# Kernel optimization log

Measured on AMD Instinct MI355X. Metric: run time of the kernel, lower is better.

## Reference

```python
import jax, jax.numpy as jnp
import numpy as np
from jax import lax

DN = ('NCHW', 'OIHW', 'NCHW')

def conv3x3(x, w, b):
    y = lax.conv_general_dilated(x, w, (1, 1), 'SAME', dimension_numbers=DN)
    return y + b[None, :, None, None]

def box_filter(x, ws):
    # depthwise WxW averaging conv, VALID after reflect pad
    C = x.shape[1]
    k = jnp.ones((C, 1, ws, ws), x.dtype) / (ws * ws)
    return lax.conv_general_dilated(x, k, (1, 1), 'VALID', feature_group_count=C,
                                    dimension_numbers=DN)

def compute_std_map(features, ws):
    N, C, H, W = features.shape
    pad = ws // 2
    fp = jnp.pad(features, ((0, 0), (0, 0), (pad, pad), (pad, pad)), mode='reflect')
    local_mean = box_filter(fp, ws)            # [N,C,H,W]
    local_mean_sq = box_filter(fp * fp, ws)
    local_var = jnp.clip(local_mean_sq - local_mean ** 2, 1e-6, None)
    if C == 4:
        cw = jax.nn.softmax(jnp.array([1.0, 1.5, 1.0, 1.5], features.dtype))
    else:
        cw = jax.nn.softmax(jnp.ones((C,), features.dtype))
    result = jnp.sum(jnp.sqrt(local_var) * cw[None, :, None, None], axis=1, keepdims=True)
    return result ** 0.8                        # [N,1,H,W]

def setup_inputs() -> dict:
    key = jax.random.key(0)
    ks = jax.random.split(key, 10)
    inp = {}
    inp['x'] = jax.random.normal(ks[0], (1, 4, 1024, 1024), jnp.float32)
    inp['w1'] = jax.random.normal(ks[1], (32, 4, 3, 3), jnp.float32) * (1.0 / np.sqrt(4 * 9))
    inp['b1'] = jax.random.normal(ks[2], (32,), jnp.float32) * 0.01
    inp['w2'] = jax.random.normal(ks[3], (16, 32, 3, 3), jnp.float32) * (1.0 / np.sqrt(32 * 9))
    inp['b2'] = jax.random.normal(ks[4], (16,), jnp.float32) * 0.01
    inp['w3'] = jax.random.normal(ks[5], (8, 16, 3, 3), jnp.float32) * (1.0 / np.sqrt(16 * 9))
    inp['b3'] = jax.random.normal(ks[6], (8,), jnp.float32) * 0.01
    inp['channel_weights'] = jnp.ones((4,), jnp.float32) / 4.0
    inp['fusion_w'] = jnp.full((1, 3, 1, 1), 1.0 / 3.0, jnp.float32) + \
        jax.random.normal(ks[7], (1, 3, 1, 1), jnp.float32) * 0.02
    inp['fusion_b'] = jnp.zeros((1,), jnp.float32)
    return inp

def reference(x, w1, b1, w2, b2, w3, b3, channel_weights, fusion_w, fusion_b):
    window_sizes = [11, 25, 49]
    # feature extractor
    f = jax.nn.leaky_relu(conv3x3(x, w1, b1), 0.2)
    f = jax.nn.leaky_relu(conv3x3(f, w2, b2), 0.2)
    f = conv3x3(f, w3, b3)                      # [B,8,H,W]
    # multi-scale std maps
    maps = jnp.concatenate([compute_std_map(f, ws) for ws in window_sizes], axis=1)  # [B,3,H,W]
    fused = jax.nn.relu(
        lax.conv_general_dilated(maps, fusion_w, (1, 1), 'VALID', dimension_numbers=DN)
        + fusion_b[None, :, None, None])        # [B,1,H,W]
    # adaptive thresholds
    std_flat = fused.reshape(-1)
    q25 = jnp.quantile(std_flat, 0.25)
    q75 = jnp.quantile(std_flat, 0.75)
    iqr75 = q75 - q25
    global_std = jnp.std(x, axis=(2, 3), keepdims=True, ddof=1)   # [B,4,1,1]
    lower = (q25 - 0.5 * iqr75) * jnp.ones_like(global_std)
    upper = (q75 + 0.5 * iqr75) * jnp.ones_like(global_std)
    gf = jnp.clip(global_std * 5.0, 0.5, 2.0)
    lower = lower * gf
    upper = upper * gf
    cwn = jax.nn.softmax(channel_weights).reshape(1, 4, 1, 1)
    channel_std = jnp.std(x * cwn, axis=(2, 3), keepdims=True, ddof=1)
    cf = jnp.clip(channel_std * 2.0, 0.8, 1.2)
    lower = lower * cf
    upper = upper * cf
    # texture mask
    q30 = jnp.quantile(std_flat, 0.3)
    q70 = jnp.quantile(std_flat, 0.7)
    lower_mean = jnp.mean(lower, axis=1, keepdims=True)           # [B,1,1,1]
    upper_mean = jnp.mean(upper, axis=1, keepdims=True)
    l_t = 0.5 * lower_mean + 0.5 * q30
    u_t = 0.5 * upper_mean + 0.5 * q70
    iqr = q70 - q30
    widen = iqr < 0.01
    l_t = jnp.where(widen, l_t - iqr, l_t)
    u_t = jnp.where(widen, u_t + iqr, u_t)
    diff = u_t - l_t
    mid0 = (l_t + u_t) / 2
    narrow = diff < 0.02
    l_t = jnp.where(narrow, mid0 - 0.01, l_t)
    u_t = jnp.where(narrow, mid0 + 0.01, u_t)
    midpoint = (l_t + u_t) / 2
    scale = u_t - l_t
    normalized = jax.nn.sigmoid(4.0 * (fused - midpoint) / scale)
    nm = jnp.mean(normalized)
    mask = jnp.where(nm > 0.65, 0.1 + 0.5 * normalized,
                     jnp.where(nm < 0.35, 0.2 + 0.5 * normalized,
                               0.15 + 0.55 * normalized))
    return mask
```

## Files before the change

kernel.cpp:

```cpp
#include <hip/hip_runtime.h>
#include <stdint.h>

constexpr int H = 1024, W = 1024;
constexpr int NPIX = H * W;
constexpr int PADM = 24;
constexpr int PROW = W + 2 * PADM;

constexpr size_t OFF_F1P   = 0;
constexpr size_t OFF_F2P   = 134217728;
constexpr size_t OFF_F3    = 0;
constexpr size_t OFF_HF    = 33554432;
constexpr size_t OFF_HF2   = 67108864;
constexpr size_t OFF_FUSED = 100663296;
constexpr size_t OFF_SMALL  = 201326592;
constexpr size_t OFF_PSTAT  = OFF_SMALL;
constexpr size_t OFF_NMSUM  = OFF_SMALL + 4096;
constexpr size_t OFF_HIST   = OFF_SMALL + 4160;
constexpr size_t OFF_RSTATE = OFF_HIST + 8192;
constexpr size_t OFF_SCAL   = OFF_RSTATE + 64;
constexpr size_t OFF_WT     = OFF_SCAL + 64;

using short8  = __attribute__((ext_vector_type(8))) short;
using short4v = __attribute__((ext_vector_type(4))) short;
using f32x4   = __attribute__((ext_vector_type(4))) float;
using uint2v  = __attribute__((ext_vector_type(2))) unsigned int;
using uint4v  = __attribute__((ext_vector_type(4))) unsigned int;

__device__ __forceinline__ int reflect1024(int j) {
    return j < 0 ? -j : (j > 1023 ? 2046 - j : j);
}
__device__ __forceinline__ unsigned short rne_bf16(float v) {
    uint32_t u = __float_as_uint(v);
    return (unsigned short)((u + 0x7FFFu + ((u >> 16) & 1u)) >> 16);
}
__device__ __forceinline__ float bf16f(unsigned short h) {
    return __uint_as_float(((uint32_t)h) << 16);
}
__device__ __forceinline__ uint32_t pack_hl(float v) {
    uint32_t u = __float_as_uint(v);
    unsigned short hh = (unsigned short)(u >> 16);
    unsigned short ll = rne_bf16(v - __uint_as_float(u & 0xFFFF0000u));
    return (uint32_t)hh | ((uint32_t)ll << 16);
}

__device__ void wfrag_body(const float* __restrict__ w, unsigned short* __restrict__ wfH,
                           unsigned short* __restrict__ wfL, int CIN, int COUT, int NF, int S,
                           int blk) {
    int total = NF * S * 512;
    int e = blk * 256 + threadIdx.x;
    if (e >= total) return;
    int j = e & 7, l = (e >> 3) & 63;
    int rest = e >> 9;
    int s = rest % S, nf = rest / S;
    int k = s * 32 + ((l >> 4) << 3) + j;
    int n = (l & 15) + 16 * nf;
    float v = 0.f;
    if (k < 9 * CIN && n < COUT) {
        int kk = k / CIN, c = k % CIN;
        int ky = kk / 3, kx = kk - ky * 3;
        v = w[((n * CIN + c) * 3 + ky) * 3 + kx];
    }
    unsigned short h = rne_bf16(v);
    wfH[e] = h;
    wfL[e] = rne_bf16(v - bf16f(h));
}

__global__ void prep_kernel(const float* __restrict__ w1, const float* __restrict__ w2,
                            const float* __restrict__ w3,
                            unsigned short* wf1H, unsigned short* wf1L,
                            unsigned short* wf2H, unsigned short* wf2L,
                            unsigned short* wf3H, unsigned short* wf3L,
                            const float* __restrict__ x, double* __restrict__ pstats,
                            double* nmsum, uint32_t* hist, uint32_t* rstate) {
    __shared__ double sb1[256], sb2[256];
    const int b = blockIdx.x, tid = threadIdx.x;
    if (b == 0) {
        for (int i = tid; i < 2048; i += 256) hist[i] = 0u;
        if (tid == 0) nmsum[0] = 0.0;
        if (tid < 8) rstate[tid] = 0u;
        if (tid < 8) {
            const uint32_t ranks[8] = {262143u, 262144u, 314572u, 314573u,
                                       734002u, 734003u, 786431u, 786432u};
            rstate[8 + tid] = ranks[tid];
        }
    } else if (b < 9) {
        wfrag_body(w1, wf1H, wf1L, 4, 32, 2, 2, b - 1);
    } else if (b < 27) {
        wfrag_body(w2, wf2H, wf2L, 32, 16, 1, 9, b - 9);
    } else if (b < 37) {
        wfrag_body(w3, wf3H, wf3L, 16, 8, 1, 5, b - 27);
    } else {
        int sb = b - 37;
        int ch = sb >> 6, blk = sb & 63;
        const float* p = x + (size_t)ch * NPIX;
        double s1 = 0.0, s2 = 0.0;
        for (int i = blk * 256 + tid; i < NPIX; i += 64 * 256) {
            double v = (double)p[i];
            s1 += v; s2 += v * v;
        }
        sb1[tid] = s1; sb2[tid] = s2;
        __syncthreads();
        for (int off = 128; off > 0; off >>= 1) {
            if (tid < off) { sb1[tid] += sb1[tid + off]; sb2[tid] += sb2[tid + off]; }
            __syncthreads();
        }
        if (tid == 0) { pstats[sb * 2] = sb1[0]; pstats[sb * 2 + 1] = sb2[0]; }
    }
}

template <int CIN, int COUT, int S, bool LEAKY, int OUT_MODE, int IN_MODE, int MINW>
__global__ __launch_bounds__(256, MINW) void mconv_kernel(
        const void* __restrict__ in,
        const unsigned short* __restrict__ wfH, const unsigned short* __restrict__ wfL,
        const float* __restrict__ bias, void* __restrict__ out) {
    constexpr int NF = (COUT + 15) / 16;
    constexpr int RS = 66 * CIN;
    constexpr int PSTR = COUT + 4;
    constexpr int STAGEB = 2 * (6 * RS) * 2;
    constexpr int EPIB = (OUT_MODE == 1) ? (4 * 64 * PSTR * 4) : (COUT * 4 * 66 * 4);
    constexpr int LBYTES = STAGEB > EPIB ? STAGEB : EPIB;
    __shared__ __align__(16) unsigned char LB[LBYTES];
    unsigned short* Ah = (unsigned short*)LB;
    unsigned short* Al = Ah + 6 * RS;

    const int tid = threadIdx.x;
    const int bx = blockIdx.x * 64, by = blockIdx.y * 4;
    const int lane = tid & 63, rw = tid >> 6;

    if constexpr (IN_MODE == 1) {
        constexpr int CPP = CIN / 4;
        constexpr int CROW = 66 * CPP;
        constexpr int TOT = 6 * CROW;
        constexpr int NLOAD = (TOT + 255) / 256;
        const uint32_t* gp = (const uint32_t*)in;

        uint4v regs[NLOAD];
#pragma unroll
        for (int k = 0; k < NLOAD; ++k) {
            int idx = tid + k * 256;
            uint4v v = uint4v{0u, 0u, 0u, 0u};
            if (idx < TOT) {
                int r = idx / CROW;
                int j = idx - r * CROW;
                int gy = by - 1 + r;
                int gx = bx - 1 + j / CPP;
                if ((unsigned)gy < 1024u && (unsigned)gx < 1024u)
                    v = *(const uint4v*)(gp + ((size_t)gy << 10) * CIN +
                                         (size_t)(bx - 1) * CIN + (size_t)j * 4);
            }
            regs[k] = v;
        }
#pragma unroll
        for (int k = 0; k < NLOAD; ++k) {
            int idx = tid + k * 256;
            if (idx < TOT) {
                int r = idx / CROW;
                int j = idx - r * CROW;
                int px = j / CPP, c0 = (j - px * CPP) * 4;
                uint32_t p0 = regs[k].x, p1 = regs[k].y, p2 = regs[k].z, p3 = regs[k].w;
                uint2v hh, ll;
                hh.x = __builtin_amdgcn_perm(p1, p0, 0x05040100u);
                hh.y = __builtin_amdgcn_perm(p3, p2, 0x05040100u);
                ll.x = __builtin_amdgcn_perm(p1, p0, 0x07060302u);
                ll.y = __builtin_amdgcn_perm(p3, p2, 0x07060302u);
                int off = r * RS + px * CIN + c0;
                *(uint2v*)(Ah + off) = hh;
                *(uint2v*)(Al + off) = ll;
            }
        }
    } else {
        constexpr int TOT = 6 * 4 * 66;
        constexpr int NLOAD = (TOT + 255) / 256;
        const float* xin = (const float*)in;
        float regs[NLOAD];
#pragma unroll
        for (int k = 0; k < NLOAD; ++k) {
            int idx = tid + k * 256;
            float v = 0.f;
            if (idx < TOT) {
                int rc  = idx / 66;
                int px  = idx - rc * 66;
                int r   = rc >> 2, c = rc & 3;
                int gy = by - 1 + r, gx = bx - 1 + px;
                if ((unsigned)gy < 1024u && (unsigned)gx < 1024u)
                    v = xin[(size_t)c * NPIX + ((size_t)gy << 10) + gx];
            }
            regs[k] = v;
        }
#pragma unroll
        for (int k = 0; k < NLOAD; ++k) {
            int idx = tid + k * 256;
            if (idx < TOT) {
                int rc  = idx / 66;
                int px  = idx - rc * 66;
                int r   = rc >> 2, c = rc & 3;
                uint32_t u = __float_as_uint(regs[k]);
                Ah[r * RS + px * CIN + c] = (unsigned short)(u >> 16);
                Al[r * RS + px * CIN + c] =
                    rne_bf16(regs[k] - __uint_as_float(u & 0xFFFF0000u));
            }
        }
    }

    short8 wh[NF][S], wl[NF][S];
#pragma unroll
    for (int nf = 0; nf < NF; ++nf)
#pragma unroll
        for (int s = 0; s < S; ++s) {
            wh[nf][s] = *(const short8*)(wfH + (size_t)((nf * S + s) * 64 + lane) * 8);
            wl[nf][s] = *(const short8*)(wfL + (size_t)((nf * S + s) * 64 + lane) * 8);
        }

    const int nidx = lane & 15;
    f32x4 acc[4][NF];
#pragma unroll
    for (int nf = 0; nf < NF; ++nf) {
        float bv = (nidx + nf * 16 < COUT) ? bias[nidx + nf * 16] : 0.f;
#pragma unroll
        for (int t = 0; t < 4; ++t) acc[t][nf] = f32x4{bv, bv, bv, bv};
    }

    __syncthreads();

    if constexpr (CIN == 32) {
        const int base = rw * RS + (lane & 15) * 32 + (lane >> 4) * 8;
        const unsigned short* pah = Ah + base;
        const unsigned short* pal = Al + base;
#pragma unroll
        for (int s = 0; s < S; ++s) {
            const int ky = s / 3, kx = s - (s / 3) * 3;
#pragma unroll
            for (int t = 0; t < 4; ++t) {
                const int off = ky * RS + kx * 32 + t * 512;
                short8 a = *(const short8*)(pah + off);
                short8 b = *(const short8*)(pal + off);
#pragma unroll
                for (int nf = 0; nf < NF; ++nf) {
                    acc[t][nf] = __builtin_amdgcn_mfma_f32_16x16x32_bf16(a, wh[nf][s], acc[t][nf], 0, 0, 0);
                    acc[t][nf] = __builtin_amdgcn_mfma_f32_16x16x32_bf16(b, wh[nf][s], acc[t][nf], 0, 0, 0);
                    acc[t][nf] = __builtin_amdgcn_mfma_f32_16x16x32_bf16(a, wl[nf][s], acc[t][nf], 0, 0, 0);
                }
            }
        }
    } else if constexpr (CIN == 16) {
        const int g23 = lane >> 5;
        const int base = rw * RS + (lane & 15) * 16 + ((lane >> 4) & 1) * 8;
#pragma unroll
        for (int s = 0; s < S; ++s) {
            const int kk0 = 2 * s, kk1 = 2 * s + 1;
            const int O0 = (kk0 / 3) * RS + (kk0 - (kk0 / 3) * 3) * 16;
            const int O1 = (kk1 <= 8) ? (kk1 / 3) * RS + (kk1 - (kk1 / 3) * 3) * 16 : 0;
            const int offs = base + (g23 ? O1 : O0);
#pragma unroll
            for (int t = 0; t < 4; ++t) {
                short8 a = *(const short8*)(Ah + offs + t * 256);
                short8 b = *(const short8*)(Al + offs + t * 256);
#pragma unroll
                for (int nf = 0; nf < NF; ++nf) {
                    acc[t][nf] = __builtin_amdgcn_mfma_f32_16x16x32_bf16(a, wh[nf][s], acc[t][nf], 0, 0, 0);
                    acc[t][nf] = __builtin_amdgcn_mfma_f32_16x16x32_bf16(b, wh[nf][s], acc[t][nf], 0, 0, 0);
                    acc[t][nf] = __builtin_amdgcn_mfma_f32_16x16x32_bf16(a, wl[nf][s], acc[t][nf], 0, 0, 0);
                }
            }
        }
    } else {
        const int base = rw * RS + (lane & 15) * 4;
        const int g2 = (lane >> 4) * 2;
#pragma unroll
        for (int s = 0; s < S; ++s) {
            int kkA = s * 8 + g2, kkB = kkA + 1;
            int kyA = (kkA * 11) >> 5; int kxA = kkA - kyA * 3;
            int poA = (kkA <= 8) ? kyA * RS + kxA * 4 : 0;
            int kyB = (kkB * 11) >> 5; int kxB = kkB - kyB * 3;
            int poB = (kkB <= 8) ? kyB * RS + kxB * 4 : 0;
#pragma unroll
            for (int t = 0; t < 4; ++t) {
                union { short4v q[2]; short8 o; } ua, ub;
                ua.q[0] = *(const short4v*)(Ah + base + poA + t * 64);
                ua.q[1] = *(const short4v*)(Ah + base + poB + t * 64);
                ub.q[0] = *(const short4v*)(Al + base + poA + t * 64);
                ub.q[1] = *(const short4v*)(Al + base + poB + t * 64);
                short8 a = ua.o, b = ub.o;
#pragma unroll
                for (int nf = 0; nf < NF; ++nf) {
                    acc[t][nf] = __builtin_amdgcn_mfma_f32_16x16x32_bf16(a, wh[nf][s], acc[t][nf], 0, 0, 0);
                    acc[t][nf] = __builtin_amdgcn_mfma_f32_16x16x32_bf16(b, wh[nf][s], acc[t][nf], 0, 0, 0);
                    acc[t][nf] = __builtin_amdgcn_mfma_f32_16x16x32_bf16(a, wl[nf][s], acc[t][nf], 0, 0, 0);
                }
            }
        }
    }

    const int mrow = (lane >> 4) * 4;
    if constexpr (OUT_MODE == 0) {
        __syncthreads();
        float* smem = (float*)LB;
        if (nidx < COUT) {
#pragma unroll
            for (int t = 0; t < 4; ++t)
#pragma unroll
                for (int j = 0; j < 4; ++j) {
                    float v = acc[t][0][j];
                    if (LEAKY) v = v >= 0.f ? v : 0.2f * v;
                    smem[(nidx * 4 + rw) * 66 + t * 16 + mrow + j] = v;
                }
        }
        __syncthreads();
        float* outp = (float*)out;
#pragma unroll
        for (int k = 0; k < COUT; ++k) {
            int i = tid + k * 256;
            int px = i & 63, r = (i >> 6) & 3, c = i >> 8;
            outp[(size_t)c * NPIX + ((size_t)(by + r) << 10) + bx + px] =
                smem[(c * 4 + r) * 66 + px];
        }
    } else {
        __syncthreads();
        uint32_t* pk = (uint32_t*)LB;
#pragma unroll
        for (int t = 0; t < 4; ++t)
#pragma unroll
            for (int nf = 0; nf < NF; ++nf)
#pragma unroll
                for (int j = 0; j < 4; ++j) {
                    float v = acc[t][nf][j];
                    if (LEAKY) v = v >= 0.f ? v : 0.2f * v;
                    int xl = t * 16 + mrow + j;
                    pk[(rw * 64 + xl) * PSTR + nf * 16 + nidx] = pack_hl(v);
                }
        __syncthreads();
        uint32_t* gp = (uint32_t*)out;
        constexpr int ROWU = 64 * COUT;
        constexpr int NU4 = 4 * ROWU / 4;
#pragma unroll
        for (int k = 0; k < (NU4 + 255) / 256; ++k) {
            int i = tid + k * 256;
            if (i < NU4) {
                int e = i * 4;
                int r = e / ROWU;
                int rem = e - r * ROWU;
                int px = rem / COUT, c = rem - px * COUT;
                uint4v val = *(const uint4v*)&pk[(r * 64 + px) * PSTR + c];
                *(uint4v*)(gp + ((size_t)(((by + r) << 10) + bx + px)) * COUT + c) = val;
            }
        }
    }
}

__global__ void hbox_kernel(const float* __restrict__ f3, float* __restrict__ hf,
                            float* __restrict__ hf2, int p) {
    const int row = blockIdx.x, ch = blockIdx.y, tid = threadIdx.x;
    const float* src = f3 + ch * NPIX + row * W;
    __shared__ float sraw[PROW];
    __shared__ float Pf[PROW + 1], Pf2[PROW + 1];
    __shared__ float wtot[4], wtot2[4];

    for (int i = tid; i < PROW; i += 256)
        sraw[i] = src[reflect1024(i - PADM)];
    __syncthreads();

    float lf[5], lf2[5];
    float sf = 0.f, sf2 = 0.f;
    const int base = tid * 5;
#pragma unroll
    for (int j = 0; j < 5; ++j) {
        int idx = base + j;
        float v = (idx < PROW) ? sraw[idx] : 0.f;
        sf += v;      lf[j] = sf;
        sf2 += v * v; lf2[j] = sf2;
    }
    const int lane = tid & 63, wid = tid >> 6;
    float tf = sf, tf2 = sf2;
#pragma unroll
    for (int off = 1; off < 64; off <<= 1) {
        float a = __shfl_up(tf, off);
        float b = __shfl_up(tf2, off);
        if (lane >= off) { tf += a; tf2 += b; }
    }
    if (lane == 63) { wtot[wid] = tf; wtot2[wid] = tf2; }
    __syncthreads();
    float bse = 0.f, bse2 = 0.f;
    for (int w2 = 0; w2 < wid; ++w2) { bse += wtot[w2]; bse2 += wtot2[w2]; }
    float ex = bse + tf - sf, ex2 = bse2 + tf2 - sf2;
    if (base <= PROW) { Pf[base] = ex; Pf2[base] = ex2; }
#pragma unroll
    for (int j = 0; j < 5; ++j) {
        int idx = base + j + 1;
        if (idx <= PROW) { Pf[idx] = ex + lf[j]; Pf2[idx] = ex2 + lf2[j]; }
    }
    __syncthreads();

    float* df  = hf  + ch * NPIX + row * W;
    float* df2 = hf2 + ch * NPIX + row * W;
    for (int x = tid; x < W; x += 256) {
        int a = x + PADM - p, b = x + PADM + p + 1;
        df[x]  = Pf[b]  - Pf[a];
        df2[x] = Pf2[b] - Pf2[a];
    }
}

constexpr int VRS = 32;
__global__ __launch_bounds__(512) void vbox_kernel(const float* __restrict__ hf,
                                                   const float* __restrict__ hf2,
                                                   float* __restrict__ fused,
                                                   const float* __restrict__ fw,
                                                   const float* __restrict__ fb,
                                                   int kidx, int p, float inv_area) {
    const int tid = threadIdx.x;
    const int colIdx = tid & 63, ch = tid >> 6;
    const int col = blockIdx.x * 64 + colIdx;
    const int r0 = blockIdx.y * VRS;
    const float* pf  = hf  + ch * NPIX + col;
    const float* pf2 = hf2 + ch * NPIX + col;

    float S1 = 0.f, S2 = 0.f;
    for (int t = -p; t <= p; ++t) {
        int rr = reflect1024(r0 + t);
        S1 += pf[rr * W];
        S2 += pf2[rr * W];
    }

    const float w = fw[kidx];
    const float bias0 = fb[0];

    __shared__ float ssq[8][8][65];
    const int jj = tid >> 6, cc = tid & 63;
    for (int rb = r0; rb < r0 + VRS; rb += 8) {
#pragma unroll
        for (int j = 0; j < 8; ++j) {
            int r = rb + j;
            float m1 = S1 * inv_area, m2 = S2 * inv_area;
            float var = fmaxf(m2 - m1 * m1, 1e-6f);
            ssq[ch][j][colIdx] = sqrtf(var);
            int radd = reflect1024(r + 1 + p), rsub = reflect1024(r - p);
            S1 += pf[radd * W] - pf[rsub * W];
            S2 += pf2[radd * W] - pf2[rsub * W];
        }
        __syncthreads();
        float a = 0.f;
#pragma unroll
        for (int c8 = 0; c8 < 8; ++c8) a += ssq[c8][jj][cc];
        float m = powf(a * 0.125f, 0.8f);
        float* fp = fused + ((size_t)(rb + jj) << 10) + blockIdx.x * 64 + cc;
        if (kidx == 0)      *fp = bias0 + w * m;
        else if (kidx == 1) *fp = *fp + w * m;
        else                *fp = fmaxf(*fp + w * m, 0.f);
        __syncthreads();
    }
}

__global__ void radix_hist_kernel(const float* __restrict__ fused, uint32_t* __restrict__ hist,
                                  const uint32_t* __restrict__ rstate, int pass) {
    __shared__ uint32_t h[8][256];
    int tid = threadIdx.x;
    for (int i = tid; i < 2048; i += 256) ((uint32_t*)h)[i] = 0u;
    __syncthreads();

    uint32_t pref[8];
#pragma unroll
    for (int r = 0; r < 8; ++r) pref[r] = rstate[r];
    uint32_t maskHi = (pass == 0) ? 0u : (0xFFFFFFFFu << (32 - 8 * pass));
    int shift = 24 - 8 * pass;

    for (int i = blockIdx.x * blockDim.x + tid; i < NPIX; i += gridDim.x * blockDim.x) {
        uint32_t u = __float_as_uint(fused[i]);
        uint32_t key = (u & 0x80000000u) ? ~u : (u | 0x80000000u);
        uint32_t bin = (key >> shift) & 0xFFu;
        if (pass == 0) {
            atomicAdd(&h[0][bin], 1u);
        } else {
#pragma unroll
            for (int r = 0; r < 8; ++r) {
                if (((key ^ pref[r]) & maskHi) == 0u)
                    atomicAdd(&h[r][bin], 1u);
            }
        }
    }
    __syncthreads();
    if (pass == 0) {
        for (int i = tid; i < 256; i += 256) {
            uint32_t v = h[0][i];
            if (v)
                for (int r = 0; r < 8; ++r) atomicAdd(&hist[r * 256 + i], v);
        }
    } else {
        for (int i = tid; i < 2048; i += 256) {
            uint32_t v = ((uint32_t*)h)[i];
            if (v) atomicAdd(&hist[i], v);
        }
    }
}

__device__ __forceinline__ float key_to_float(uint32_t k) {
    uint32_t u = (k & 0x80000000u) ? (k & 0x7FFFFFFFu) : ~k;
    return __uint_as_float(u);
}

__global__ void radix_scan_kernel(uint32_t* __restrict__ hist, uint32_t* __restrict__ rstate,
                                  int pass, const double* __restrict__ pstats,
                                  const float* __restrict__ cw, float* __restrict__ scal) {
    int tid = threadIdx.x;
    int shift = 24 - 8 * pass;
    const int lane = tid & 63, wv = tid >> 6;
    __shared__ uint32_t wsum[4];
    __shared__ uint32_t fkey[8];
    for (int r = 0; r < 8; ++r) {
        uint32_t c = hist[r * 256 + tid];
        uint32_t sc = c;
#pragma unroll
        for (int off = 1; off < 64; off <<= 1) {
            uint32_t t = __shfl_up(sc, off);
            if (lane >= off) sc += t;
        }
        if (lane == 63) wsum[wv] = sc;
        __syncthreads();
        uint32_t base = 0;
        for (int w2 = 0; w2 < wv; ++w2) base += wsum[w2];
        uint32_t incl = base + sc, excl = incl - c;
        uint32_t lr = rstate[8 + r];
        if (lr >= excl && lr < incl) {
            uint32_t nk = rstate[r] | (((uint32_t)tid) << shift);
            rstate[r] = nk;
            rstate[8 + r] = lr - excl;
            if (pass == 3) fkey[r] = nk;
        }
        hist[r * 256 + tid] = 0u;
        __syncthreads();
    }

    if (pass == 3) {
        double s1 = pstats[2 * tid], s2 = pstats[2 * tid + 1];
#pragma unroll
        for (int off = 32; off > 0; off >>= 1) {
            s1 += __shfl_down(s1, off);
            s2 += __shfl_down(s2, off);
        }
        __shared__ double gs[4][2];
        if ((tid & 63) == 0) { gs[tid >> 6][0] = s1; gs[tid >> 6][1] = s2; }
        __syncthreads();
        if (tid == 0) {
            float v[8];
#pragma unroll
            for (int r = 0; r < 8; ++r) v[r] = key_to_float(fkey[r]);
            float q25 = v[0] + 0.75f * (v[1] - v[0]);
            float q30 = v[2] + 0.5f * (v[3] - v[2]);
            float q70 = v[4] + 0.5f * (v[5] - v[4]);
            float q75 = v[6] + 0.25f * (v[7] - v[6]);

            const double N = (double)NPIX;
            float gstd[4];
#pragma unroll
            for (int c = 0; c < 4; ++c) {
                double a1 = gs[c][0], a2 = gs[c][1];
                double var = (a2 - a1 * a1 / N) / (N - 1.0);
                gstd[c] = (float)sqrt(var > 0.0 ? var : 0.0);
            }
            float m = fmaxf(fmaxf(cw[0], cw[1]), fmaxf(cw[2], cw[3]));
            float e0 = expf(cw[0] - m), e1 = expf(cw[1] - m);
            float e2 = expf(cw[2] - m), e3 = expf(cw[3] - m);
            float se = e0 + e1 + e2 + e3;
            float cwn[4] = {e0 / se, e1 / se, e2 / se, e3 / se};

            float iqr75 = q75 - q25;
            float low0 = q25 - 0.5f * iqr75;
            float up0  = q75 + 0.5f * iqr75;
            float lsum = 0.f, usum = 0.f;
#pragma unroll
            for (int c = 0; c < 4; ++c) {
                float gf = fminf(fmaxf(gstd[c] * 5.f, 0.5f), 2.f);
                float cs = cwn[c] * gstd[c];
                float cf = fminf(fmaxf(cs * 2.f, 0.8f), 1.2f);
                lsum += low0 * gf * cf;
                usum += up0 * gf * cf;
            }
            float lmean = 0.25f * lsum, umean = 0.25f * usum;
            float l_t = 0.5f * lmean + 0.5f * q30;
            float u_t = 0.5f * umean + 0.5f * q70;
            float iqr = q70 - q30;
            if (iqr < 0.01f) { l_t -= iqr; u_t += iqr; }
            float diff = u_t - l_t;
            float mid0 = 0.5f * (l_t + u_t);
            if (diff < 0.02f) { l_t = mid0 - 0.01f; u_t = mid0 + 0.01f; }
            scal[0] = 0.5f * (l_t + u_t);
            scal[1] = u_t - l_t;
        }
    }
}

__global__ void sigmoid_kernel(const float* __restrict__ fused, const float* __restrict__ scal,
                               double* __restrict__ nmsum) {
    float mid = scal[0], sc = scal[1];
    float inv = 4.0f / sc;
    float local = 0.f;
    for (int i = blockIdx.x * blockDim.x + threadIdx.x; i < NPIX; i += gridDim.x * blockDim.x) {
        float t = (fused[i] - mid) * inv;
        local += 1.0f / (1.0f + expf(-t));
    }
    __shared__ float red[256];
    red[threadIdx.x] = local;
    __syncthreads();
    for (int off = 128; off > 0; off >>= 1) {
        if (threadIdx.x < off) red[threadIdx.x] += red[threadIdx.x + off];
        __syncthreads();
    }
    if (threadIdx.x == 0) atomicAdd(nmsum, (double)red[0]);
}

__global__ void final_kernel(const float* __restrict__ fused, const float* __restrict__ scal,
                             const double* __restrict__ nmsum, float* __restrict__ out) {
    float nm = (float)(nmsum[0] / (double)NPIX);
    float a, b;
    if (nm > 0.65f)      { a = 0.10f; b = 0.50f; }
    else if (nm < 0.35f) { a = 0.20f; b = 0.50f; }
    else                 { a = 0.15f; b = 0.55f; }
    float mid = scal[0], inv = 4.0f / scal[1];
    for (int i = blockIdx.x * blockDim.x + threadIdx.x; i < NPIX; i += gridDim.x * blockDim.x) {
        float t = (fused[i] - mid) * inv;
        float n = 1.0f / (1.0f + expf(-t));
        out[i] = a + b * n;
    }
}

extern "C" void kernel_launch(void* const* d_in, const int* in_sizes, int n_in,
                              void* d_out, int out_size, void* d_ws, size_t ws_size,
                              hipStream_t stream) {
    const float* x   = (const float*)d_in[0];
    const float* w1  = (const float*)d_in[1];
    const float* b1  = (const float*)d_in[2];
    const float* w2  = (const float*)d_in[3];
    const float* b2  = (const float*)d_in[4];
    const float* w3  = (const float*)d_in[5];
    const float* b3  = (const float*)d_in[6];
    const float* cw  = (const float*)d_in[7];
    const float* fw  = (const float*)d_in[8];
    const float* fb  = (const float*)d_in[9];

    char* ws = (char*)d_ws;
    uint32_t* f1p = (uint32_t*)(ws + OFF_F1P);
    uint32_t* f2p = (uint32_t*)(ws + OFF_F2P);
    float* f3    = (float*)(ws + OFF_F3);
    float* hf    = (float*)(ws + OFF_HF);
    float* hf2   = (float*)(ws + OFF_HF2);
    float* fused = (float*)(ws + OFF_FUSED);
    double* pstats = (double*)(ws + OFF_PSTAT);
    double* nmsum  = (double*)(ws + OFF_NMSUM);
    uint32_t* hist   = (uint32_t*)(ws + OFF_HIST);
    uint32_t* rstate = (uint32_t*)(ws + OFF_RSTATE);
    float* scal = (float*)(ws + OFF_SCAL);
    unsigned short* wf1H = (unsigned short*)(ws + OFF_WT);
    unsigned short* wf1L = wf1H + 2048;
    unsigned short* wf2H = wf1L + 2048;
    unsigned short* wf2L = wf2H + 4608;
    unsigned short* wf3H = wf2L + 4608;
    unsigned short* wf3L = wf3H + 2560;

    prep_kernel<<<293, 256, 0, stream>>>(w1, w2, w3, wf1H, wf1L, wf2H, wf2L, wf3H, wf3L,
                                         x, pstats, nmsum, hist, rstate);

    dim3 cgrid(16, 256);
    mconv_kernel<4, 32, 2, true, 1, 0, 4><<<cgrid, 256, 0, stream>>>(
        x, wf1H, wf1L, b1, f1p);
    mconv_kernel<32, 16, 9, true, 1, 1, 3><<<cgrid, 256, 0, stream>>>(
        f1p, wf2H, wf2L, b2, f2p);
    mconv_kernel<16, 8, 5, false, 0, 1, 4><<<cgrid, 256, 0, stream>>>(
        f2p, wf3H, wf3L, b3, f3);

    const int wss[3] = {11, 25, 49};
    for (int k = 0; k < 3; ++k) {
        int p = wss[k] / 2;
        float inv_area = 1.0f / (float)(wss[k] * wss[k]);
        hbox_kernel<<<dim3(H, 8), 256, 0, stream>>>(f3, hf, hf2, p);
        vbox_kernel<<<dim3(W / 64, H / VRS), 512, 0, stream>>>(hf, hf2, fused, fw, fb,
                                                               k, p, inv_area);
    }

    for (int pass = 0; pass < 4; ++pass) {
        radix_hist_kernel<<<512, 256, 0, stream>>>(fused, hist, rstate, pass);
        radix_scan_kernel<<<1, 256, 0, stream>>>(hist, rstate, pass, pstats, cw, scal);
    }

    sigmoid_kernel<<<1024, 256, 0, stream>>>(fused, scal, nmsum);
    final_kernel<<<1024, 256, 0, stream>>>(fused, scal, nmsum, (float*)d_out);
}
```

Measured before the change: 359.6 us.

## Share one horizontal prefix-sum pass across all three box-filter window sizes

Replaces the per-window horizontal box kernel with a single kernel that writes row-wise prefix sums of f3 and f3^2 once. The vertical kernel then gets each horizontal window sum by differencing the prefix array, handling reflect padding algebraically at the edges. This removes two of the three horizontal passes and their 64MB write traffic. The cost is that every vertical update now needs four gathered loads instead of two, with extra branching near the borders. Summing prefix values over a whole row may also lose some float precision.

```diff
diff --git a/kernel.cpp b/kernel.cpp
--- a/kernel.cpp
+++ b/kernel.cpp
@@ -3,15 +3,15 @@
 
 constexpr int H = 1024, W = 1024;
 constexpr int NPIX = H * W;
-constexpr int PADM = 24;
-constexpr int PROW = W + 2 * PADM;
+constexpr int PRSU = 1028;
 
 constexpr size_t OFF_F1P   = 0;
 constexpr size_t OFF_F2P   = 134217728;
 constexpr size_t OFF_F3    = 0;
-constexpr size_t OFF_HF    = 33554432;
-constexpr size_t OFF_HF2   = 67108864;
-constexpr size_t OFF_FUSED = 100663296;
+constexpr size_t PBYTES    = 8ull * 1024 * PRSU * 4;
+constexpr size_t OFF_P1    = 33554432;
+constexpr size_t OFF_P2    = OFF_P1 + PBYTES;
+constexpr size_t OFF_FUSED = OFF_P2 + PBYTES;
 constexpr size_t OFF_SMALL  = 201326592;
 constexpr size_t OFF_PSTAT  = OFF_SMALL;
 constexpr size_t OFF_NMSUM  = OFF_SMALL + 4096;
@@ -347,25 +347,22 @@
     }
 }
 
-__global__ void hbox_kernel(const float* __restrict__ f3, float* __restrict__ hf,
-                            float* __restrict__ hf2, int p) {
+__global__ void hboxp_kernel(const float* __restrict__ f3, float* __restrict__ P1,
+                             float* __restrict__ P2) {
     const int row = blockIdx.x, ch = blockIdx.y, tid = threadIdx.x;
-    const float* src = f3 + ch * NPIX + row * W;
-    __shared__ float sraw[PROW];
-    __shared__ float Pf[PROW + 1], Pf2[PROW + 1];
+    const float* src = f3 + (size_t)ch * NPIX + (size_t)row * W;
+    __shared__ float sraw[1024];
     __shared__ float wtot[4], wtot2[4];
 
-    for (int i = tid; i < PROW; i += 256)
-        sraw[i] = src[reflect1024(i - PADM)];
+    for (int i = tid; i < 1024; i += 256) sraw[i] = src[i];
     __syncthreads();
 
-    float lf[5], lf2[5];
+    const int base = tid * 4;
+    float lf[4], lf2[4];
     float sf = 0.f, sf2 = 0.f;
-    const int base = tid * 5;
-#pragma unroll
-    for (int j = 0; j < 5; ++j) {
-        int idx = base + j;
-        float v = (idx < PROW) ? sraw[idx] : 0.f;
+#pragma unroll
+    for (int j = 0; j < 4; ++j) {
+        float v = sraw[base + j];
         sf += v;      lf[j] = sf;
         sf2 += v * v; lf2[j] = sf2;
     }
@@ -382,42 +379,50 @@
     float bse = 0.f, bse2 = 0.f;
     for (int w2 = 0; w2 < wid; ++w2) { bse += wtot[w2]; bse2 += wtot2[w2]; }
     float ex = bse + tf - sf, ex2 = bse2 + tf2 - sf2;
-    if (base <= PROW) { Pf[base] = ex; Pf2[base] = ex2; }
-#pragma unroll
-    for (int j = 0; j < 5; ++j) {
-        int idx = base + j + 1;
-        if (idx <= PROW) { Pf[idx] = ex + lf[j]; Pf2[idx] = ex2 + lf2[j]; }
-    }
-    __syncthreads();
-
-    float* df  = hf  + ch * NPIX + row * W;
-    float* df2 = hf2 + ch * NPIX + row * W;
-    for (int x = tid; x < W; x += 256) {
-        int a = x + PADM - p, b = x + PADM + p + 1;
-        df[x]  = Pf[b]  - Pf[a];
-        df2[x] = Pf2[b] - Pf2[a];
+
+    float* d1 = P1 + ((size_t)ch * 1024 + row) * PRSU;
+    float* d2 = P2 + ((size_t)ch * 1024 + row) * PRSU;
+    if (tid == 0) { d1[0] = 0.f; d2[0] = 0.f; }
+#pragma unroll
+    for (int j = 0; j < 4; ++j) {
+        d1[base + j + 1] = ex + lf[j];
+        d2[base + j + 1] = ex2 + lf2[j];
     }
 }
 
 constexpr int VRS = 32;
-__global__ __launch_bounds__(512) void vbox_kernel(const float* __restrict__ hf,
-                                                   const float* __restrict__ hf2,
-                                                   float* __restrict__ fused,
-                                                   const float* __restrict__ fw,
-                                                   const float* __restrict__ fb,
-                                                   int kidx, int p, float inv_area) {
+__global__ __launch_bounds__(512) void vboxp_kernel(const float* __restrict__ P1,
+                                                    const float* __restrict__ P2,
+                                                    float* __restrict__ fused,
+                                                    const float* __restrict__ fw,
+                                                    const float* __restrict__ fb,
+                                                    int kidx, int p, float inv_area) {
     const int tid = threadIdx.x;
     const int colIdx = tid & 63, ch = tid >> 6;
-    const int col = blockIdx.x * 64 + colIdx;
+    const int x = blockIdx.x * 64 + colIdx;
     const int r0 = blockIdx.y * VRS;
-    const float* pf  = hf  + ch * NPIX + col;
-    const float* pf2 = hf2 + ch * NPIX + col;
+    const float* B1 = P1 + (size_t)ch * 1024 * PRSU;
+    const float* B2 = P2 + (size_t)ch * 1024 * PRSU;
+
+    const int lo = x - p, hi = x + p;
+    const int iLo = lo > 0 ? lo : 0;
+    const int iHi = (hi < 1023 ? hi : 1023) + 1;
+    const bool lrefl = lo < 0, rrefl = hi > 1023;
+    const int lIdx = 1 - lo;
+    const int rIdx = 2046 - hi;
+
+    auto hs = [&](const float* P) -> float {
+        float s = P[iHi] - P[iLo];
+        if (lrefl) s += P[lIdx] - P[1];
+        if (rrefl) s += P[1023] - P[rIdx];
+        return s;
+    };
 
     float S1 = 0.f, S2 = 0.f;
     for (int t = -p; t <= p; ++t) {
         int rr = reflect1024(r0 + t);
-        S1 += pf[rr * W];
-        S2 += pf2[rr * W];
+        S1 += hs(B1 + (size_t)rr * PRSU);
+        S2 += hs(B2 + (size_t)rr * PRSU);
     }
 
     const float w = fw[kidx];
@@ -433,8 +438,8 @@
             float var = fmaxf(m2 - m1 * m1, 1e-6f);
             ssq[ch][j][colIdx] = sqrtf(var);
             int radd = reflect1024(r + 1 + p), rsub = reflect1024(r - p);
-            S1 += pf[radd * W] - pf[rsub * W];
-            S2 += pf2[radd * W] - pf2[rsub * W];
+            S1 += hs(B1 + (size_t)radd * PRSU) - hs(B1 + (size_t)rsub * PRSU);
+            S2 += hs(B2 + (size_t)radd * PRSU) - hs(B2 + (size_t)rsub * PRSU);
         }
         __syncthreads();
         float a = 0.f;
@@ -639,8 +644,8 @@
     uint32_t* f1p = (uint32_t*)(ws + OFF_F1P);
     uint32_t* f2p = (uint32_t*)(ws + OFF_F2P);
     float* f3    = (float*)(ws + OFF_F3);
-    float* hf    = (float*)(ws + OFF_HF);
-    float* hf2   = (float*)(ws + OFF_HF2);
+    float* P1    = (float*)(ws + OFF_P1);
+    float* P2    = (float*)(ws + OFF_P2);
     float* fused = (float*)(ws + OFF_FUSED);
     double* pstats = (double*)(ws + OFF_PSTAT);
     double* nmsum  = (double*)(ws + OFF_NMSUM);
@@ -665,13 +670,13 @@
     mconv_kernel<16, 8, 5, false, 0, 1, 4><<<cgrid, 256, 0, stream>>>(
         f2p, wf3H, wf3L, b3, f3);
 
+    hboxp_kernel<<<dim3(H, 8), 256, 0, stream>>>(f3, P1, P2);
     const int wss[3] = {11, 25, 49};
     for (int k = 0; k < 3; ++k) {
         int p = wss[k] / 2;
         float inv_area = 1.0f / (float)(wss[k] * wss[k]);
-        hbox_kernel<<<dim3(H, 8), 256, 0, stream>>>(f3, hf, hf2, p);
-        vbox_kernel<<<dim3(W / 64, H / VRS), 512, 0, stream>>>(hf, hf2, fused, fw, fb,
-                                                               k, p, inv_area);
+        vboxp_kernel<<<dim3(W / 64, H / VRS), 512, 0, stream>>>(P1, P2, fused, fw, fb,
+                                                                k, p, inv_area);
     }
 
     for (int pass = 0; pass < 4; ++pass) {
```

New measurement: 555.0 us. +54.3%, slower.
